# Kernel optimization log

Hardware: AMD Instinct MI355X
Metric: run time of the kernel (lower is better)

Reference implementation:

```python
import jax, jax.numpy as jnp
import numpy as np

H = 8          # n_heads
M = 16         # max_dist
U = 512        # n_units
DH = U // H    # d_head
EPS = 1e-3     # keras LayerNormalization default epsilon
NEG = -2.0**32 + 1.0


def _rel_table(pe, T):
    # pe: [2M+1, DH]; returns [T, T, DH] with rel[i, j] = pe[clip(j - i, -M, M) + M]
    i = jnp.arange(T)
    idx = jnp.clip(i[None, :] - i[:, None], -M, M) + M
    return pe[idx]


def _split_heads(x):
    # [B, T, U] -> [H*B, T, DH]  (head-major, matching tf.concat(tf.split(x, H, 2), 0))
    B, T, _ = x.shape
    return x.reshape(B, T, H, DH).transpose(2, 0, 1, 3).reshape(H * B, T, DH)


def _merge_heads(x, B):
    # [H*B, T, DH] -> [B, T, U]
    T = x.shape[1]
    return x.reshape(H, B, T, DH).transpose(1, 2, 0, 3).reshape(B, T, U)


def setup_inputs() -> dict:
    key = jax.random.key(0)
    ks = jax.random.split(key, 10)
    B, T = 8, 1024
    s = 1.0 / np.sqrt(U)
    inp = {
        'q': jax.random.normal(ks[0], (B, T, U), jnp.float32),
        'k': jax.random.normal(ks[1], (B, T, U), jnp.float32),
        'v': jax.random.normal(ks[2], (B, T, U), jnp.float32),
        'Wq': jax.random.normal(ks[3], (U, U), jnp.float32) * s,
        'bq': jnp.zeros((U,), jnp.float32),
        'Wk': jax.random.normal(ks[4], (U, U), jnp.float32) * s,
        'bk': jnp.zeros((U,), jnp.float32),
        'Wv': jax.random.normal(ks[5], (U, U), jnp.float32) * s,
        'bv': jnp.zeros((U,), jnp.float32),
        'Wo': jax.random.normal(ks[6], (U, U), jnp.float32) * s,
        'bo': jnp.zeros((U,), jnp.float32),
        'gamma': jnp.ones((U,), jnp.float32),
        'beta': jnp.zeros((U,), jnp.float32),
        'pe_k': jax.random.normal(ks[7], (2 * M + 1, DH), jnp.float32) * 0.05,
        'pe_v': jax.random.normal(ks[8], (2 * M + 1, DH), jnp.float32) * 0.05,
    }
    return inp


def reference(q, k, v, Wq, bq, Wk, bk, Wv, bv, Wo, bo, gamma, beta, pe_k, pe_v):
    B, T, _ = q.shape
    relu = jax.nn.relu
    q_emb = relu(q @ Wq + bq)
    k_emb = relu(k @ Wk + bk)
    v_emb = relu(v @ Wv + bv)
    qh = _split_heads(q_emb)   # [HB, T, DH]
    kh = _split_heads(k_emb)
    vh = _split_heads(v_emb)

    attn = jnp.einsum('btd,bsd->bts', qh, kh)
    rel_k = _rel_table(pe_k, T)                       # [T, T, DH]
    attn = attn + jnp.einsum('btd,tsd->bts', qh, rel_k)
    attn = attn / jnp.asarray(DH, attn.dtype) ** 0.5

    causal = jnp.tril(jnp.ones((T, T), jnp.bool_))
    attn = jnp.where(causal[None], attn, jnp.asarray(NEG, attn.dtype))
    w = jax.nn.softmax(attn, axis=-1)

    out = jnp.einsum('bts,bsd->btd', w, vh)
    rel_v = _rel_table(pe_v, T)
    out = out + jnp.einsum('bts,tsd->btd', w, rel_v)

    out = _merge_heads(out, B)                        # [B, T, U]
    out = relu(out @ Wo + bo)
    out = out + q

    mu = jnp.mean(out, axis=-1, keepdims=True)
    var = jnp.mean(jnp.square(out - mu), axis=-1, keepdims=True)
    return (out - mu) * jax.lax.rsqrt(var + EPS) * gamma + beta
```

## Files before the change

kernel.cpp:

```cpp
#include <hip/hip_runtime.h>
#include <hip/hip_bf16.h>

#define T_SEQ 1024
#define U_DIM 512
#define LN_EPS 1e-3f

typedef float  f32x4  __attribute__((ext_vector_type(4)));
typedef short  bf16x8 __attribute__((ext_vector_type(8)));

__device__ __forceinline__ unsigned short f2bf(float f) {
    union { float f; unsigned u; } x; x.f = f;
    unsigned r = x.u + 0x7fffu + ((x.u >> 16) & 1u);
    return (unsigned short)(r >> 16);
}
__device__ __forceinline__ float b2f(short s) {
    union { unsigned u; float f; } x; x.u = ((unsigned)(unsigned short)s) << 16;
    return x.f;
}
__device__ __forceinline__ int packbf(float a, float b) {
    return (int)((unsigned)f2bf(a) | ((unsigned)f2bf(b) << 16));
}
__device__ __forceinline__ void async_copy16(void* lds, const void* g) {
    __builtin_amdgcn_global_load_lds((const __attribute__((address_space(1))) void*)g,
                                     (__attribute__((address_space(3))) void*)lds, 16, 0, 0);
}

#define WAITV(N) asm volatile("s_waitcnt vmcnt(" #N ")" ::: "memory")

__global__ __launch_bounds__(256) void conv_bf16(
        const float* __restrict__ q, const float* __restrict__ k, const float* __restrict__ v,
        short* __restrict__ qb, short* __restrict__ kb, short* __restrict__ vb) {
    const size_t off = ((size_t)blockIdx.x * 256 + threadIdx.x) * 8;
#pragma unroll
    for (int z = 0; z < 3; ++z) {
        const float* src = (z == 0) ? q : (z == 1) ? k : v;
        short* dst = (z == 0) ? qb : (z == 1) ? kb : vb;
        float4 a = *(const float4*)(src + off);
        float4 b = *(const float4*)(src + off + 4);
        int4 o;
        o.x = packbf(a.x, a.y);
        o.y = packbf(a.z, a.w);
        o.z = packbf(b.x, b.y);
        o.w = packbf(b.z, b.w);
        *(int4*)(dst + off) = o;
    }
}

__global__ __launch_bounds__(256) void prep_wt(
        const float* __restrict__ Wq, const float* __restrict__ Wk,
        const float* __restrict__ Wv, const float* __restrict__ Wo,
        short* __restrict__ wt) {
    __shared__ float Ws[64][65];
    const int bid = blockIdx.x, t = threadIdx.x;
    const int z = bid >> 6, tile = bid & 63;
    const float* W = (z == 0) ? Wq : (z == 1) ? Wk : (z == 2) ? Wv : Wo;
    short* Wt = wt + (size_t)z * 262144;
    const int k0 = (tile >> 3) * 64, n0 = (tile & 7) * 64;
    {
        const int kr = t >> 2, cs = (t & 3) * 16;
        const float4* src = (const float4*)(W + (size_t)(k0 + kr) * 512 + n0 + cs);
#pragma unroll
        for (int i = 0; i < 4; ++i) {
            float4 vv = src[i];
            Ws[kr][cs + 4 * i + 0] = vv.x;
            Ws[kr][cs + 4 * i + 1] = vv.y;
            Ws[kr][cs + 4 * i + 2] = vv.z;
            Ws[kr][cs + 4 * i + 3] = vv.w;
        }
    }
    __syncthreads();
    {
        const int nr = t >> 2, ks = (t & 3) * 16;
        int4 w0, w1;
        w0.x = packbf(Ws[ks + 0][nr], Ws[ks + 1][nr]);
        w0.y = packbf(Ws[ks + 2][nr], Ws[ks + 3][nr]);
        w0.z = packbf(Ws[ks + 4][nr], Ws[ks + 5][nr]);
        w0.w = packbf(Ws[ks + 6][nr], Ws[ks + 7][nr]);
        w1.x = packbf(Ws[ks + 8][nr], Ws[ks + 9][nr]);
        w1.y = packbf(Ws[ks + 10][nr], Ws[ks + 11][nr]);
        w1.z = packbf(Ws[ks + 12][nr], Ws[ks + 13][nr]);
        w1.w = packbf(Ws[ks + 14][nr], Ws[ks + 15][nr]);
        short* dst = Wt + (size_t)(n0 + nr) * 512 + k0 + ks;
        *(int4*)dst = w0;
        *(int4*)(dst + 8) = w1;
    }
}

template <int OUT, int BM, int BN>
__global__ __launch_bounds__(256) void gemm_mfma(
        const void* __restrict__ A0, const void* __restrict__ A1, const void* __restrict__ A2,
        const short* __restrict__ Wt0, const short* __restrict__ Wt1, const short* __restrict__ Wt2,
        const float* __restrict__ b0p, const float* __restrict__ b1p, const float* __restrict__ b2p,
        const float* __restrict__ resid,
        void* __restrict__ O0, void* __restrict__ O1, void* __restrict__ O2) {
    constexpr int ASZ = BM * 32;
    constexpr int BSZ = BN * 32;
    constexpr int TSZ = ASZ + BSZ;
    constexpr int NA  = BM / 16;
    constexpr int NB  = BN / 16;
    constexpr int MW  = BM / 64;
    constexpr int NW  = 4 / MW;
    constexpr int AJ  = BN / (16 * NW);
    static_assert(NA + NB == 12, "3 loads per wave");
    __shared__ short Ls[4 * TSZ];

    const int z = blockIdx.z;
    const void* Av = (z == 0) ? A0 : (z == 1) ? A1 : A2;
    const short* Wz = (z == 0) ? Wt0 : (z == 1) ? Wt1 : Wt2;
    const float* bz = (z == 0) ? b0p : (z == 1) ? b1p : b2p;
    void* Ov = (z == 0) ? O0 : (z == 1) ? O1 : O2;

    const int tid = threadIdx.x;
    const int m0 = blockIdx.x * BM, n0 = blockIdx.y * BN;
    const int w = tid >> 6, lane = tid & 63;
    const int n15 = lane & 15, g = lane >> 4;
    const int mh = w / NW, nh = w % NW;

    f32x4 acc[4][AJ];
#pragma unroll
    for (int i = 0; i < 4; ++i)
#pragma unroll
        for (int j = 0; j < AJ; ++j) acc[i][j] = (f32x4){0.f, 0.f, 0.f, 0.f};

    const short* gsrc[3];
    int loff[3];
#pragma unroll
    for (int cl = 0; cl < 3; ++cl) {
        const int cid = w * 3 + cl;
        if (cid < NA) {
            gsrc[cl] = (const short*)Av + (size_t)(m0 + cid * 16 + n15) * 512 + g * 8;
            loff[cl] = cid * 512;
        } else {
            const int c2 = cid - NA;
            gsrc[cl] = Wz + (size_t)(n0 + c2 * 16 + n15) * 512 + g * 8;
            loff[cl] = ASZ + c2 * 512;
        }
    }

#define STAGE(CK, BUF)                                                                   \
    do {                                                                                 \
        _Pragma("unroll")                                                                \
        for (int cl = 0; cl < 3; ++cl)                                                   \
            async_copy16(Ls + (BUF) * TSZ + loff[cl], gsrc[cl] + (CK) * 32);             \
    } while (0)

    STAGE(0, 0);
    STAGE(1, 1);
    STAGE(2, 2);

    for (int ck = 0; ck < 16; ++ck) {
        if (ck < 14) WAITV(6);
        else if (ck == 14) WAITV(3);
        else WAITV(0);
        __builtin_amdgcn_s_barrier();
        __builtin_amdgcn_sched_barrier(0);
        if (ck + 3 <= 15) STAGE(ck + 3, (ck + 3) & 3);
        const int cb = ck & 3;
        bf16x8 af[4], bfv[AJ];
#pragma unroll
        for (int i = 0; i < 4; ++i)
            af[i] = *(const bf16x8*)(Ls + cb * TSZ + (mh * 4 + i) * 512 + lane * 8);
#pragma unroll
        for (int j = 0; j < AJ; ++j)
            bfv[j] = *(const bf16x8*)(Ls + cb * TSZ + ASZ + (nh * AJ + j) * 512 + lane * 8);
#pragma unroll
        for (int i = 0; i < 4; ++i)
#pragma unroll
            for (int j = 0; j < AJ; ++j)
                acc[i][j] = __builtin_amdgcn_mfma_f32_16x16x32_bf16(af[i], bfv[j], acc[i][j], 0, 0, 0);
    }
#undef STAGE

    const int mbase = m0 + mh * 64 + g * 4;
    const int nbase = n0 + nh * (AJ * 16) + n15;
    const bool even = (n15 & 1) == 0;
    float bj[AJ];
#pragma unroll
    for (int j = 0; j < AJ; ++j) bj[j] = bz[nbase + j * 16];

#pragma unroll
    for (int i = 0; i < 4; ++i) {
        const int mrow = mbase + i * 16;
#pragma unroll
        for (int j = 0; j < AJ; ++j) {
            const int ncol = nbase + j * 16;
            f32x4 a = acc[i][j];
            float v0 = fmaxf(a[0] + bj[j], 0.f);
            float v1 = fmaxf(a[1] + bj[j], 0.f);
            float v2 = fmaxf(a[2] + bj[j], 0.f);
            float v3 = fmaxf(a[3] + bj[j], 0.f);
            if (OUT == 0) {
                unsigned t01 = (unsigned)packbf(v0, v1);
                unsigned t23 = (unsigned)packbf(v2, v3);
                unsigned x01 = (unsigned)__shfl_xor((int)t01, 1, 64);
                unsigned x23 = (unsigned)__shfl_xor((int)t23, 1, 64);
                short* Oz = (short*)Ov;
                if (even) {
                    unsigned d0 = (t01 & 0xffffu) | (x01 << 16);
                    unsigned d1 = (t01 >> 16) | (x01 & 0xffff0000u);
                    *(unsigned*)(Oz + (size_t)(mrow + 0) * 512 + ncol) = d0;
                    *(unsigned*)(Oz + (size_t)(mrow + 1) * 512 + ncol) = d1;
                } else {
                    unsigned d2 = (x23 & 0xffffu) | (t23 << 16);
                    unsigned d3 = (x23 >> 16) | (t23 & 0xffff0000u);
                    *(unsigned*)(Oz + (size_t)(mrow + 2) * 512 + ncol - 1) = d2;
                    *(unsigned*)(Oz + (size_t)(mrow + 3) * 512 + ncol - 1) = d3;
                }
            } else {
                float x0 = __shfl_xor(v0, 1, 64);
                float x1 = __shfl_xor(v1, 1, 64);
                float x2 = __shfl_xor(v2, 1, 64);
                float x3 = __shfl_xor(v3, 1, 64);
                float* Oz = (float*)Ov;
                if (even) {
                    float2 r0 = *(const float2*)(resid + (size_t)(mrow + 0) * 512 + ncol);
                    float2 r1 = *(const float2*)(resid + (size_t)(mrow + 1) * 512 + ncol);
                    *(float2*)(Oz + (size_t)(mrow + 0) * 512 + ncol) = make_float2(v0 + r0.x, x0 + r0.y);
                    *(float2*)(Oz + (size_t)(mrow + 1) * 512 + ncol) = make_float2(v1 + r1.x, x1 + r1.y);
                } else {
                    float2 r2 = *(const float2*)(resid + (size_t)(mrow + 2) * 512 + ncol - 1);
                    float2 r3 = *(const float2*)(resid + (size_t)(mrow + 3) * 512 + ncol - 1);
                    *(float2*)(Oz + (size_t)(mrow + 2) * 512 + ncol - 1) = make_float2(x2 + r2.x, v2 + r2.y);
                    *(float2*)(Oz + (size_t)(mrow + 3) * 512 + ncol - 1) = make_float2(x3 + r3.x, v3 + r3.y);
                }
            }
        }
    }
}

__global__ __launch_bounds__(256) void attn_mfma(
        const short* __restrict__ qe, const short* __restrict__ ke,
        const short* __restrict__ ve, const float* __restrict__ pe_k,
        float* __restrict__ ml, short* __restrict__ ao) {
    __shared__ short Kc[2 * 4096];
    __shared__ short Vc[2 * 4096];
    __shared__ float qpeS[4 * 16 * 17];

    const int tid = threadIdx.x;
    const int bid = blockIdx.x;
    const int q4 = bid >> 8, r4 = bid & 3;
    const int rank = (q4 < 2) ? (r4 + 4 * q4) : (15 - (r4 + 4 * (q4 - 2)));
    const int hb = (bid >> 2) & 63;
    const int tt = 15 - rank;
    const int h = hb >> 3, b = hb & 7;
    const int w = tid >> 6, lane = tid & 63;
    const int g = lane >> 4, n15 = lane & 15;
    const int sp = tid & 31, dbase = (tid >> 5) * 8;
    float* qpeW = qpeS + w * (16 * 17);

    const size_t rowbase = (size_t)b * T_SEQ;

    int qn = 0;
    bf16x8 Bq[2];
    float qpe0 = 0.f;
    float m_r = -3.0e38f, l_r = 0.f;
    f32x4 oacc[4];

#define SETUP(TILE)                                                                      \
    do {                                                                                 \
        qn = (TILE) * 64 + w * 16;                                                       \
        _Pragma("unroll")                                                                \
        for (int kh = 0; kh < 2; ++kh) {                                                 \
            bf16x8 t = *(const bf16x8*)(qe + (rowbase + qn + n15) * U_DIM + h * 64 + kh * 32 + g * 8); \
            _Pragma("unroll")                                                            \
            for (int i2 = 0; i2 < 8; ++i2) {                                             \
                unsigned short u = (unsigned short)t[i2];                                \
                t[i2] = (short)(((u & 0x7f80u) > 0x0180u) ? (unsigned short)(u - 0x0180u) \
                                                          : (unsigned short)(u & 0x8000u)); \
            }                                                                            \
            Bq[kh] = t;                                                                  \
        }                                                                                \
        f32x4 qa[2];                                                                     \
        qa[0] = (f32x4){0.f, 0.f, 0.f, 0.f};                                             \
        qa[1] = (f32x4){0.f, 0.f, 0.f, 0.f};                                             \
        _Pragma("unroll")                                                                \
        for (int mt = 0; mt < 2; ++mt)                                                   \
        _Pragma("unroll")                                                                \
        for (int kh = 0; kh < 2; ++kh) {                                                 \
            const float* src = pe_k + (mt * 16 + n15) * 64 + kh * 32 + g * 8;            \
            float4 f0 = *(const float4*)src;                                             \
            float4 f1 = *(const float4*)(src + 4);                                       \
            bf16x8 fr;                                                                   \
            fr[0] = (short)f2bf(f0.x); fr[1] = (short)f2bf(f0.y);                        \
            fr[2] = (short)f2bf(f0.z); fr[3] = (short)f2bf(f0.w);                        \
            fr[4] = (short)f2bf(f1.x); fr[5] = (short)f2bf(f1.y);                        \
            fr[6] = (short)f2bf(f1.z); fr[7] = (short)f2bf(f1.w);                        \
            qa[mt] = __builtin_amdgcn_mfma_f32_16x16x32_bf16(fr, Bq[kh], qa[mt], 0, 0, 0); \
        }                                                                                \
        _Pragma("unroll")                                                                \
        for (int mt = 0; mt < 2; ++mt)                                                   \
        _Pragma("unroll")                                                                \
        for (int r = 0; r < 4; ++r) {                                                    \
            const int ri = mt * 16 + 4 * g + r;                                          \
            if (ri <= 16) qpeW[n15 * 17 + ri] = qa[mt][r];                               \
        }                                                                                \
        qpe0 = qpeW[n15 * 17];                                                           \
        m_r = -3.0e38f; l_r = 0.f;                                                       \
        _Pragma("unroll")                                                                \
        for (int dt = 0; dt < 4; ++dt) oacc[dt] = (f32x4){0.f, 0.f, 0.f, 0.f};           \
    } while (0)

#define STAGE_K(S, BUF)                                                                  \
    do {                                                                                 \
        _Pragma("unroll")                                                                \
        for (int j = 0; j < 2; ++j) {                                                    \
            const int cc = w * 2 + j, kh = cc >> 2, mt = cc & 3;                         \
            const short* gp = ke + (rowbase + (S) + mt * 16 + n15) * U_DIM + h * 64 + kh * 32 + g * 8; \
            async_copy16(Kc + (BUF) * 4096 + cc * 512, gp);                              \
        }                                                                                \
    } while (0)

#define LOAD_V(S)                                                                        \
    do {                                                                                 \
        const short* r0 = ve + (rowbase + (S) + 2 * sp) * U_DIM + h * 64 + dbase;        \
        vx = *(const bf16x8*)r0;                                                         \
        vy = *(const bf16x8*)(r0 + U_DIM);                                               \
    } while (0)

#define STORE_V(BUF)                                                                     \
    do {                                                                                 \
        const int vkh = sp >> 4, vg = (sp & 15) >> 2, vj = (sp & 3) * 2;                 \
        _Pragma("unroll")                                                                \
        for (int i = 0; i < 8; ++i) {                                                    \
            const int d = dbase + i;                                                     \
            int pv = (int)((unsigned short)vx[i]) | (((int)(unsigned short)vy[i]) << 16);\
            *(int*)(Vc + (BUF) * 4096 + (vkh * 4 + (d >> 4)) * 512 + ((d & 15) + 16 * vg) * 8 + vj) = pv; \
        }                                                                                \
    } while (0)

    SETUP(tt);
    bf16x8 vx, vy;
    STAGE_K(0, 0);
    LOAD_V(0);
    STORE_V(0);

    for (int gs = 0; gs <= tt; ++gs) {
        const int cb = gs & 1, nb = cb ^ 1;
        const int s0 = gs * 64;
        __syncthreads();
        if (gs < tt) {
            STAGE_K((gs + 1) * 64, nb);
            LOAD_V((gs + 1) * 64);
        }

        {
            int cls[4];
#pragma unroll
            for (int mt = 0; mt < 4; ++mt) {
                const int slo = s0 + mt * 16;
                cls[mt] = (slo > qn + 15) ? 0 : ((slo + 31 < qn) ? 1 : 2);
            }
            f32x4 c[4];
#pragma unroll
            for (int mt = 0; mt < 4; ++mt) c[mt] = (f32x4){0.f, 0.f, 0.f, 0.f};
#pragma unroll
            for (int mt = 0; mt < 4; ++mt) {
                if (!cls[mt]) continue;
#pragma unroll
                for (int kh = 0; kh < 2; ++kh) {
                    bf16x8 ak = *(const bf16x8*)(Kc + cb * 4096 + (kh * 4 + mt) * 512 + lane * 8);
                    c[mt] = __builtin_amdgcn_mfma_f32_16x16x32_bf16(ak, Bq[kh], c[mt], 0, 0, 0);
                }
            }

            const int qg = qn + n15;
            float sc[4][4];
            float pmax = -3.0e38f;
#pragma unroll
            for (int mt = 0; mt < 4; ++mt) {
                if (cls[mt] == 0) {
#pragma unroll
                    for (int r = 0; r < 4; ++r) sc[mt][r] = -3.0e38f;
                } else if (cls[mt] == 1) {
#pragma unroll
                    for (int r = 0; r < 4; ++r) {
                        sc[mt][r] = c[mt][r] + qpe0;
                        pmax = fmaxf(pmax, sc[mt][r]);
                    }
                } else {
#pragma unroll
                    for (int r = 0; r < 4; ++r) {
                        const int sg = s0 + mt * 16 + 4 * g + r;
                        const int dlt = sg - qg;
                        if (dlt <= 0) {
                            const int ri = (dlt < -16) ? 0 : (dlt + 16);
                            sc[mt][r] = c[mt][r] + qpeW[n15 * 17 + ri];
                            pmax = fmaxf(pmax, sc[mt][r]);
                        } else {
                            sc[mt][r] = -3.0e38f;
                        }
                    }
                }
            }
            pmax = fmaxf(pmax, __shfl_xor(pmax, 16, 64));
            pmax = fmaxf(pmax, __shfl_xor(pmax, 32, 64));

            const bool resc = __any(pmax > m_r + 8.0f);
            float mnew = m_r, alpha = 1.0f;
            if (resc) {
                mnew = fmaxf(m_r, pmax);
                alpha = __expf(m_r - mnew);
            }
            float p[4][4];
            float psum = 0.f;
#pragma unroll
            for (int mt = 0; mt < 4; ++mt)
#pragma unroll
            for (int r = 0; r < 4; ++r) {
                const float pv = (cls[mt] == 0) ? 0.f : __expf(sc[mt][r] - mnew);
                p[mt][r] = pv;
                psum += pv;
            }
            psum += __shfl_xor(psum, 16, 64);
            psum += __shfl_xor(psum, 32, 64);
            l_r = l_r * alpha + psum;
            m_r = mnew;

            int pk01[4], pk23[4];
#pragma unroll
            for (int mt = 0; mt < 4; ++mt) {
                pk01[mt] = packbf(p[mt][0], p[mt][1]);
                pk23[mt] = packbf(p[mt][2], p[mt][3]);
            }
            const int srcA = ((g & 1) * 2) * 16 + n15;
            const int srcB = srcA + 16;
            const bool selHi = (g >> 1) != 0;
            if (resc) {
                float aO[4];
#pragma unroll
                for (int r = 0; r < 4; ++r) aO[r] = __shfl(alpha, 4 * g + r, 64);
#pragma unroll
                for (int dt = 0; dt < 4; ++dt)
#pragma unroll
                for (int r = 0; r < 4; ++r) oacc[dt][r] *= aO[r];
            }
#pragma unroll
            for (int kh = 0; kh < 2; ++kh) {
                if (cls[2 * kh] == 0 && cls[2 * kh + 1] == 0) continue;
                const int a0l = __shfl(pk01[2 * kh], srcA, 64);
                const int a0h = __shfl(pk01[2 * kh + 1], srcA, 64);
                const int a1l = __shfl(pk23[2 * kh], srcA, 64);
                const int a1h = __shfl(pk23[2 * kh + 1], srcA, 64);
                const int a2l = __shfl(pk01[2 * kh], srcB, 64);
                const int a2h = __shfl(pk01[2 * kh + 1], srcB, 64);
                const int a3l = __shfl(pk23[2 * kh], srcB, 64);
                const int a3h = __shfl(pk23[2 * kh + 1], srcB, 64);
                union { int i[4]; bf16x8 v; } au;
                au.i[0] = selHi ? a0h : a0l;
                au.i[1] = selHi ? a1h : a1l;
                au.i[2] = selHi ? a2h : a2l;
                au.i[3] = selHi ? a3h : a3l;
#pragma unroll
                for (int dt = 0; dt < 4; ++dt) {
                    bf16x8 bv = *(const bf16x8*)(Vc + cb * 4096 + (kh * 4 + dt) * 512 + lane * 8);
                    oacc[dt] = __builtin_amdgcn_mfma_f32_16x16x32_bf16(au.v, bv, oacc[dt], 0, 0, 0);
                }
            }
        }

        if (gs < tt) STORE_V(nb);
    }

    if (g == 0)
        *(float2*)(ml + ((size_t)hb * T_SEQ + qn + n15) * 2) = make_float2(m_r, l_r);
#pragma unroll
    for (int r = 0; r < 4; ++r) {
        const float lq = __shfl(l_r, 4 * g + r, 64);
        const float linv = 1.0f / lq;
        short* dst = ao + (rowbase + qn + 4 * g + r) * U_DIM + h * 64 + n15;
#pragma unroll
        for (int dt = 0; dt < 4; ++dt)
            dst[dt * 16] = (short)f2bf(oacc[dt][r] * linv);
    }
#undef SETUP
#undef STAGE_K
#undef LOAD_V
#undef STORE_V
}

__global__ __launch_bounds__(256) void band_relv(
        const short* __restrict__ qe, const short* __restrict__ ke,
        const float* __restrict__ pe_k, const float* __restrict__ pe_v,
        const float* __restrict__ ml, short* __restrict__ ao) {
    __shared__ float pek[17 * 64];
    __shared__ float pev[17 * 64];
    const int tb = blockIdx.x, hb = blockIdx.y;
    const int h = hb >> 3, b = hb & 7;
    const int tid = threadIdx.x;
    for (int i = tid; i < 17 * 64; i += 256) {
        pek[i] = b2f((short)f2bf(pe_k[i]));
        pev[i] = pe_v[i];
    }
    __syncthreads();

    const int t = tb * 64 + (tid >> 2);
    const int p = (tid & 3) * 16;
    const short* qp = qe + (size_t)(b * T_SEQ + t) * U_DIM + h * 64 + p;
    bf16x8 qa = *(const bf16x8*)qp, qb2 = *(const bf16x8*)(qp + 8);
    float qv[16];
#pragma unroll
    for (int i = 0; i < 8; ++i) { qv[i] = b2f(qa[i]); qv[8 + i] = b2f(qb2[i]); }

    float dots[17];
#pragma unroll
    for (int ri = 0; ri < 17; ++ri) {
        const int s = t - 16 + ri;
        float acc = 0.f;
        if (s >= 0) {
            const short* kp = ke + (size_t)(b * T_SEQ + s) * U_DIM + h * 64 + p;
            bf16x8 ka = *(const bf16x8*)kp, kb2 = *(const bf16x8*)(kp + 8);
#pragma unroll
            for (int d = 0; d < 8; ++d) {
                acc += qv[d] * b2f(ka[d]);
                acc += qv[8 + d] * b2f(kb2[d]);
            }
#pragma unroll
            for (int d = 0; d < 16; ++d) acc += qv[d] * pek[ri * 64 + p + d];
        }
        dots[ri] = acc;
    }
#pragma unroll
    for (int ri = 0; ri < 17; ++ri) {
        dots[ri] += __shfl_xor(dots[ri], 1, 64);
        dots[ri] += __shfl_xor(dots[ri], 2, 64);
    }

    const float2 mlv = *(const float2*)(ml + ((size_t)hb * T_SEQ + t) * 2);
    const float m = mlv.x, linv = 1.0f / mlv.y;
    float wv[17];
    float wsum = 0.f;
#pragma unroll
    for (int ri = 0; ri < 17; ++ri) {
        const int s = t - 16 + ri;
        const float wr = (s >= 0) ? __expf(dots[ri] * 0.125f - m) * linv : 0.f;
        wv[ri] = wr;
        wsum += wr;
    }
    wv[0] += 1.0f - wsum;

    float relv[16];
#pragma unroll
    for (int d = 0; d < 16; ++d) relv[d] = 0.f;
#pragma unroll
    for (int ri = 0; ri < 17; ++ri)
#pragma unroll
        for (int d = 0; d < 16; ++d) relv[d] += wv[ri] * pev[ri * 64 + p + d];

    short* op = ao + (size_t)(b * T_SEQ + t) * U_DIM + h * 64 + p;
    bf16x8 a0 = *(const bf16x8*)op, a1 = *(const bf16x8*)(op + 8);
    int4 o0, o1;
    o0.x = packbf(b2f(a0[0]) + relv[0],  b2f(a0[1]) + relv[1]);
    o0.y = packbf(b2f(a0[2]) + relv[2],  b2f(a0[3]) + relv[3]);
    o0.z = packbf(b2f(a0[4]) + relv[4],  b2f(a0[5]) + relv[5]);
    o0.w = packbf(b2f(a0[6]) + relv[6],  b2f(a0[7]) + relv[7]);
    o1.x = packbf(b2f(a1[0]) + relv[8],  b2f(a1[1]) + relv[9]);
    o1.y = packbf(b2f(a1[2]) + relv[10], b2f(a1[3]) + relv[11]);
    o1.z = packbf(b2f(a1[4]) + relv[12], b2f(a1[5]) + relv[13]);
    o1.w = packbf(b2f(a1[6]) + relv[14], b2f(a1[7]) + relv[15]);
    *(int4*)op = o0;
    *(int4*)(op + 8) = o1;
}

__global__ __launch_bounds__(256) void ln_kernel(float* __restrict__ io,
                                                 const float* __restrict__ gamma,
                                                 const float* __restrict__ beta) {
    const int row = blockIdx.x * 4 + (threadIdx.x >> 6);
    const int lane = threadIdx.x & 63;
    float* rp = io + (size_t)row * 512 + lane * 8;
    float4 a = *(const float4*)rp;
    float4 c = *(const float4*)(rp + 4);
    float v[8] = {a.x, a.y, a.z, a.w, c.x, c.y, c.z, c.w};

    float s = v[0] + v[1] + v[2] + v[3] + v[4] + v[5] + v[6] + v[7];
#pragma unroll
    for (int off = 1; off < 64; off <<= 1) s += __shfl_xor(s, off, 64);
    const float mu = s * (1.0f / 512.0f);

    float sq = 0.f;
#pragma unroll
    for (int i = 0; i < 8; ++i) { v[i] -= mu; sq += v[i] * v[i]; }
#pragma unroll
    for (int off = 1; off < 64; off <<= 1) sq += __shfl_xor(sq, off, 64);
    const float rs = rsqrtf(sq * (1.0f / 512.0f) + LN_EPS);

    const float4 g0 = *(const float4*)(gamma + lane * 8);
    const float4 g1 = *(const float4*)(gamma + lane * 8 + 4);
    const float4 b0 = *(const float4*)(beta + lane * 8);
    const float4 b1 = *(const float4*)(beta + lane * 8 + 4);
    float4 o0, o1;
    o0.x = v[0] * rs * g0.x + b0.x;
    o0.y = v[1] * rs * g0.y + b0.y;
    o0.z = v[2] * rs * g0.z + b0.z;
    o0.w = v[3] * rs * g0.w + b0.w;
    o1.x = v[4] * rs * g1.x + b1.x;
    o1.y = v[5] * rs * g1.y + b1.y;
    o1.z = v[6] * rs * g1.z + b1.z;
    o1.w = v[7] * rs * g1.w + b1.w;
    *(float4*)rp = o0;
    *(float4*)(rp + 4) = o1;
}

extern "C" void kernel_launch(void* const* d_in, const int* in_sizes, int n_in,
                              void* d_out, int out_size, void* d_ws, size_t ws_size,
                              hipStream_t stream) {
    const float* q     = (const float*)d_in[0];
    const float* k     = (const float*)d_in[1];
    const float* v     = (const float*)d_in[2];
    const float* Wq    = (const float*)d_in[3];
    const float* bq    = (const float*)d_in[4];
    const float* Wk    = (const float*)d_in[5];
    const float* bk    = (const float*)d_in[6];
    const float* Wv    = (const float*)d_in[7];
    const float* bv    = (const float*)d_in[8];
    const float* Wo    = (const float*)d_in[9];
    const float* bo    = (const float*)d_in[10];
    const float* gamma = (const float*)d_in[11];
    const float* beta  = (const float*)d_in[12];
    const float* pe_k  = (const float*)d_in[13];
    const float* pe_v  = (const float*)d_in[14];
    float* out = (float*)d_out;

    char* base = (char*)d_ws;
    short* qe = (short*)(base);
    short* ke = (short*)(base + (((size_t)8) << 20));
    short* ve = (short*)(base + (((size_t)16) << 20));
    short* ao = (short*)(base + (((size_t)24) << 20));
    short* wt = (short*)(base + (((size_t)32) << 20));
    float* ml = (float*)(base + (((size_t)34) << 20));
    short* qb = (short*)(base + (((size_t)36) << 20));
    short* kb = (short*)(base + (((size_t)44) << 20));
    short* vb = (short*)(base + (((size_t)52) << 20));
    short* wtq = wt, *wtk = wt + 262144, *wtv = wt + 2 * 262144, *wto = wt + 3 * 262144;

    prep_wt<<<dim3(256), 256, 0, stream>>>(Wq, Wk, Wv, Wo, wt);
    conv_bf16<<<dim3(2048), 256, 0, stream>>>(q, k, v, qb, kb, vb);
    gemm_mfma<0, 128, 64><<<dim3(64, 8, 3), 256, 0, stream>>>(
        qb, kb, vb, wtq, wtk, wtv, bq, bk, bv, nullptr, qe, ke, ve);
    attn_mfma<<<dim3(1024), 256, 0, stream>>>(qe, ke, ve, pe_k, ml, ao);
    band_relv<<<dim3(16, 64), 256, 0, stream>>>(qe, ke, pe_k, pe_v, ml, ao);
    gemm_mfma<1, 64, 128><<<dim3(128, 4, 1), 256, 0, stream>>>(
        ao, ao, ao, wto, wto, wto, bo, bo, bo, q, out, out, out);
    ln_kernel<<<dim3(2048), 256, 0, stream>>>(out, gamma, beta);
}
```

Before: 248.4 us.

## Merge prep kernels, retile output GEMM, tune attention softmax and MFMA priority

Fuses the weight-transpose and bf16 conversion kernels into one launch. The output GEMM moves to 64x64 tiles with twice as many blocks, and the load-per-wave count and waitcnt values are generalised to fit. In attention, the softmax exponent uses exp2 with a precomputed scaled max, probabilities are packed to bf16 with a hardware convert instruction, and MFMA sections are wrapped in s_setprio. Together these cut launch overhead, raise occupancy for the small GEMM, and trim ALU work in the softmax, at the cost of a smaller per-block tile and more blocks.

Result: no change. 252.6 us (+1.7%).

```diff
diff --git a/kernel.cpp b/kernel.cpp
--- a/kernel.cpp
+++ b/kernel.cpp
@@ -4,6 +4,7 @@
 #define T_SEQ 1024
 #define U_DIM 512
 #define LN_EPS 1e-3f
+#define LOG2E 1.44269504f
 
 typedef float  f32x4  __attribute__((ext_vector_type(4)));
 typedef short  bf16x8 __attribute__((ext_vector_type(8)));
@@ -27,31 +28,31 @@
 
 #define WAITV(N) asm volatile("s_waitcnt vmcnt(" #N ")" ::: "memory")
 
-__global__ __launch_bounds__(256) void conv_bf16(
+__global__ __launch_bounds__(256) void prep_all(
+        const float* __restrict__ Wq, const float* __restrict__ Wk,
+        const float* __restrict__ Wv, const float* __restrict__ Wo,
+        short* __restrict__ wt,
         const float* __restrict__ q, const float* __restrict__ k, const float* __restrict__ v,
         short* __restrict__ qb, short* __restrict__ kb, short* __restrict__ vb) {
-    const size_t off = ((size_t)blockIdx.x * 256 + threadIdx.x) * 8;
-#pragma unroll
-    for (int z = 0; z < 3; ++z) {
-        const float* src = (z == 0) ? q : (z == 1) ? k : v;
-        short* dst = (z == 0) ? qb : (z == 1) ? kb : vb;
-        float4 a = *(const float4*)(src + off);
-        float4 b = *(const float4*)(src + off + 4);
-        int4 o;
-        o.x = packbf(a.x, a.y);
-        o.y = packbf(a.z, a.w);
-        o.z = packbf(b.x, b.y);
-        o.w = packbf(b.z, b.w);
-        *(int4*)(dst + off) = o;
-    }
-}
-
-__global__ __launch_bounds__(256) void prep_wt(
-        const float* __restrict__ Wq, const float* __restrict__ Wk,
-        const float* __restrict__ Wv, const float* __restrict__ Wo,
-        short* __restrict__ wt) {
     __shared__ float Ws[64][65];
     const int bid = blockIdx.x, t = threadIdx.x;
+    if (bid >= 256) {
+        const size_t off = ((size_t)(bid - 256) * 256 + t) * 8;
+#pragma unroll
+        for (int z = 0; z < 3; ++z) {
+            const float* src = (z == 0) ? q : (z == 1) ? k : v;
+            short* dst = (z == 0) ? qb : (z == 1) ? kb : vb;
+            float4 a = *(const float4*)(src + off);
+            float4 b = *(const float4*)(src + off + 4);
+            int4 o;
+            o.x = packbf(a.x, a.y);
+            o.y = packbf(a.z, a.w);
+            o.z = packbf(b.x, b.y);
+            o.w = packbf(b.z, b.w);
+            *(int4*)(dst + off) = o;
+        }
+        return;
+    }
     const int z = bid >> 6, tile = bid & 63;
     const float* W = (z == 0) ? Wq : (z == 1) ? Wk : (z == 2) ? Wv : Wo;
     short* Wt = wt + (size_t)z * 262144;
@@ -101,7 +102,8 @@
     constexpr int MW  = BM / 64;
     constexpr int NW  = 4 / MW;
     constexpr int AJ  = BN / (16 * NW);
-    static_assert(NA + NB == 12, "3 loads per wave");
+    constexpr int LPW = (NA + NB) / 4;
+    static_assert((NA + NB) % 4 == 0, "cells divisible by waves");
     __shared__ short Ls[4 * TSZ];
 
     const int z = blockIdx.z;
@@ -122,11 +124,11 @@
 #pragma unroll
         for (int j = 0; j < AJ; ++j) acc[i][j] = (f32x4){0.f, 0.f, 0.f, 0.f};
 
-    const short* gsrc[3];
-    int loff[3];
-#pragma unroll
-    for (int cl = 0; cl < 3; ++cl) {
-        const int cid = w * 3 + cl;
+    const short* gsrc[LPW];
+    int loff[LPW];
+#pragma unroll
+    for (int cl = 0; cl < LPW; ++cl) {
+        const int cid = w * LPW + cl;
         if (cid < NA) {
             gsrc[cl] = (const short*)Av + (size_t)(m0 + cid * 16 + n15) * 512 + g * 8;
             loff[cl] = cid * 512;
@@ -140,7 +142,7 @@
 #define STAGE(CK, BUF)                                                                   \
     do {                                                                                 \
         _Pragma("unroll")                                                                \
-        for (int cl = 0; cl < 3; ++cl)                                                   \
+        for (int cl = 0; cl < LPW; ++cl)                                                 \
             async_copy16(Ls + (BUF) * TSZ + loff[cl], gsrc[cl] + (CK) * 32);             \
     } while (0)
 
@@ -149,9 +151,13 @@
     STAGE(2, 2);
 
     for (int ck = 0; ck < 16; ++ck) {
-        if (ck < 14) WAITV(6);
-        else if (ck == 14) WAITV(3);
-        else WAITV(0);
+        if (ck < 14) {
+            if constexpr (LPW == 3) WAITV(6); else WAITV(4);
+        } else if (ck == 14) {
+            if constexpr (LPW == 3) WAITV(3); else WAITV(2);
+        } else {
+            WAITV(0);
+        }
         __builtin_amdgcn_s_barrier();
         __builtin_amdgcn_sched_barrier(0);
         if (ck + 3 <= 15) STAGE(ck + 3, (ck + 3) & 3);
@@ -253,7 +259,7 @@
     int qn = 0;
     bf16x8 Bq[2];
     float qpe0 = 0.f;
-    float m_r = -3.0e38f, l_r = 0.f;
+    float m_r = -1.0e38f, l_r = 0.f, m2 = -1.4427e38f;
     f32x4 oacc[4];
 
 #define SETUP(TILE)                                                                      \
@@ -295,7 +301,7 @@
             if (ri <= 16) qpeW[n15 * 17 + ri] = qa[mt][r];                               \
         }                                                                                \
         qpe0 = qpeW[n15 * 17];                                                           \
-        m_r = -3.0e38f; l_r = 0.f;                                                       \
+        m_r = -1.0e38f; l_r = 0.f; m2 = -1.4427e38f;                                     \
         _Pragma("unroll")                                                                \
         for (int dt = 0; dt < 4; ++dt) oacc[dt] = (f32x4){0.f, 0.f, 0.f, 0.f};           \
     } while (0)
@@ -353,6 +359,7 @@
             f32x4 c[4];
 #pragma unroll
             for (int mt = 0; mt < 4; ++mt) c[mt] = (f32x4){0.f, 0.f, 0.f, 0.f};
+            __builtin_amdgcn_s_setprio(1);
 #pragma unroll
             for (int mt = 0; mt < 4; ++mt) {
                 if (!cls[mt]) continue;
@@ -362,6 +369,7 @@
                     c[mt] = __builtin_amdgcn_mfma_f32_16x16x32_bf16(ak, Bq[kh], c[mt], 0, 0, 0);
                 }
             }
+            __builtin_amdgcn_s_setprio(0);
 
             const int qg = qn + n15;
             float sc[4][4];
@@ -396,10 +404,12 @@
             pmax = fmaxf(pmax, __shfl_xor(pmax, 32, 64));
 
             const bool resc = __any(pmax > m_r + 8.0f);
-            float mnew = m_r, alpha = 1.0f;
+            float alpha = 1.0f;
             if (resc) {
-                mnew = fmaxf(m_r, pmax);
+                const float mnew = fmaxf(m_r, pmax);
                 alpha = __expf(m_r - mnew);
+                m_r = mnew;
+                m2 = mnew * LOG2E;
             }
             float p[4][4];
             float psum = 0.f;
@@ -407,20 +417,20 @@
             for (int mt = 0; mt < 4; ++mt)
 #pragma unroll
             for (int r = 0; r < 4; ++r) {
-                const float pv = (cls[mt] == 0) ? 0.f : __expf(sc[mt][r] - mnew);
+                const float pv = (cls[mt] == 0) ? 0.f
+                                : exp2f(fmaf(sc[mt][r], LOG2E, -m2));
                 p[mt][r] = pv;
                 psum += pv;
             }
             psum += __shfl_xor(psum, 16, 64);
             psum += __shfl_xor(psum, 32, 64);
             l_r = l_r * alpha + psum;
-            m_r = mnew;
 
             int pk01[4], pk23[4];
 #pragma unroll
             for (int mt = 0; mt < 4; ++mt) {
-                pk01[mt] = packbf(p[mt][0], p[mt][1]);
-                pk23[mt] = packbf(p[mt][2], p[mt][3]);
+                asm("v_cvt_pk_bf16_f32 %0, %1, %2" : "=v"(pk01[mt]) : "v"(p[mt][0]), "v"(p[mt][1]));
+                asm("v_cvt_pk_bf16_f32 %0, %1, %2" : "=v"(pk23[mt]) : "v"(p[mt][2]), "v"(p[mt][3]));
             }
             const int srcA = ((g & 1) * 2) * 16 + n15;
             const int srcB = srcA + 16;
@@ -450,11 +460,13 @@
                 au.i[1] = selHi ? a1h : a1l;
                 au.i[2] = selHi ? a2h : a2l;
                 au.i[3] = selHi ? a3h : a3l;
+                __builtin_amdgcn_s_setprio(1);
 #pragma unroll
                 for (int dt = 0; dt < 4; ++dt) {
                     bf16x8 bv = *(const bf16x8*)(Vc + cb * 4096 + (kh * 4 + dt) * 512 + lane * 8);
                     oacc[dt] = __builtin_amdgcn_mfma_f32_16x16x32_bf16(au.v, bv, oacc[dt], 0, 0, 0);
                 }
+                __builtin_amdgcn_s_setprio(0);
             }
         }
 
@@ -632,13 +644,12 @@
     short* vb = (short*)(base + (((size_t)52) << 20));
     short* wtq = wt, *wtk = wt + 262144, *wtv = wt + 2 * 262144, *wto = wt + 3 * 262144;
 
-    prep_wt<<<dim3(256), 256, 0, stream>>>(Wq, Wk, Wv, Wo, wt);
-    conv_bf16<<<dim3(2048), 256, 0, stream>>>(q, k, v, qb, kb, vb);
+    prep_all<<<dim3(2304), 256, 0, stream>>>(Wq, Wk, Wv, Wo, wt, q, k, v, qb, kb, vb);
     gemm_mfma<0, 128, 64><<<dim3(64, 8, 3), 256, 0, stream>>>(
         qb, kb, vb, wtq, wtk, wtv, bq, bk, bv, nullptr, qe, ke, ve);
     attn_mfma<<<dim3(1024), 256, 0, stream>>>(qe, ke, ve, pe_k, ml, ao);
     band_relv<<<dim3(16, 64), 256, 0, stream>>>(qe, ke, pe_k, pe_v, ml, ao);
-    gemm_mfma<1, 64, 128><<<dim3(128, 4, 1), 256, 0, stream>>>(
+    gemm_mfma<1, 64, 64><<<dim3(128, 8, 1), 256, 0, stream>>>(
         ao, ao, ao, wto, wto, wto, bo, bo, bo, q, out, out, out);
     ln_kernel<<<dim3(2048), 256, 0, stream>>>(out, gamma, beta);
 }
```
